# Kernel tuning notes

Hardware: AMD Instinct MI355X
Metric: run time of the kernel (lower is better)

The kernel has to match this reference:

```python
import jax, jax.numpy as jnp
import numpy as np

B, T = 64, 512          # batch, seq_len
D = 512                 # model_size / LSTM hidden
V = 256                 # vocab_size
R, W, M = 4, 16, 5      # read_heads, cell_size, nr_cells
RW = R * W
IFC = R * W + 3 * W + 5 * R + 3   # DNC interface vector size = 135
EPS = 1e-6
CLIP = 20.0


def setup_inputs():
    ks = jax.random.split(jax.random.key(0), 12)
    s = 0.05
    f32 = jnp.float32
    return {
        'tokens':   jax.random.randint(ks[0], (B, T), 0, V, dtype=jnp.int32),
        'emb':      jax.random.normal(ks[1], (V, D), f32),
        'lstm_Wi0': jax.random.normal(ks[2], (4 * D, D + RW), f32) * s,
        'lstm_Wh0': jax.random.normal(ks[3], (4 * D, D), f32) * s,
        'lstm_b0':  jnp.zeros((4 * D,), f32),
        'lstm_Wi1': jax.random.normal(ks[4], (4 * D, D), f32) * s,
        'lstm_Wh1': jax.random.normal(ks[5], (4 * D, D), f32) * s,
        'lstm_b1':  jnp.zeros((4 * D,), f32),
        'W_if':     jax.random.normal(ks[6], (IFC, D), f32) * s,
        'b_if':     jnp.zeros((IFC,), f32),
        'W_out':    jax.random.normal(ks[7], (D, D + RW), f32) * s,
        'b_out':    jnp.zeros((D,), f32),
        'W_fc':     jax.random.normal(ks[8], (V, D), f32) * s,
        'b_fc':     jnp.zeros((V,), f32),
    }


def _cosine(mem, keys):
    # mem (B,M,W), keys (B,K,W) -> (B,K,M) batchwise cosine similarity
    mn = mem / (jnp.linalg.norm(mem, axis=2, keepdims=True) + EPS)
    kn = keys / (jnp.linalg.norm(keys, axis=2, keepdims=True) + EPS)
    return jnp.einsum('bkw,bmw->bkm', kn, mn)


def _allocate(usage):
    # DNC allocation weighting via sort + exclusive cumprod, then unsort
    u = EPS + (1.0 - EPS) * usage                           # (B,M)
    idx = jnp.argsort(u, axis=1)                            # ascending usage
    sorted_u = jnp.take_along_axis(u, idx, axis=1)
    prod_excl = jnp.cumprod(
        jnp.concatenate([jnp.ones_like(u[:, :1]), sorted_u], axis=1), axis=1)[:, :-1]
    alloc_sorted = (1.0 - sorted_u) * prod_excl
    inv = jnp.argsort(idx, axis=1)                          # reverse permutation
    return jnp.take_along_axis(alloc_sorted, inv, axis=1)


def _dnc_forward(tokens, emb, lstm_Wi0, lstm_Wh0, lstm_b0,
                 lstm_Wi1, lstm_Wh1, lstm_b1, W_if, b_if,
                 W_out, b_out, W_fc, b_fc):
    x = emb[tokens]                                         # (B,T,D)
    eye_mask = 1.0 - jnp.eye(M, dtype=x.dtype)

    def lstm_cell(xin, h, c, Wi, Wh, b):
        g = xin @ Wi.T + h @ Wh.T + b
        i, f, gg, o = jnp.split(g, 4, axis=1)               # torch gate order i,f,g,o
        c2 = jax.nn.sigmoid(f) * c + jax.nn.sigmoid(i) * jnp.tanh(gg)
        h2 = jax.nn.sigmoid(o) * jnp.tanh(c2)
        return h2, c2

    def step(carry, x_t):
        h0, c0, h1, c1, mem, link, prec, rw_p, ww_p, usage, last_read = carry
        xin = jnp.concatenate([x_t, last_read], axis=1)     # (B, D+RW)
        nh0, nc0 = lstm_cell(xin, h0, c0, lstm_Wi0, lstm_Wh0, lstm_b0)
        nh1, nc1 = lstm_cell(nh0, h1, c1, lstm_Wi1, lstm_Wh1, lstm_b1)
        out = jnp.clip(nh1, -CLIP, CLIP)
        xi = out @ W_if.T + b_if                            # (B, IFC)

        o = 0
        read_keys = jnp.tanh(xi[:, :RW]).reshape(-1, R, W); o = RW
        read_str  = jax.nn.softplus(xi[:, o:o + R]); o += R
        write_key = jnp.tanh(xi[:, o:o + W]); o += W
        write_str = jax.nn.softplus(xi[:, o]); o += 1
        erase     = jax.nn.sigmoid(xi[:, o:o + W]); o += W
        write_vec = jnp.tanh(xi[:, o:o + W]); o += W
        free_g    = jax.nn.sigmoid(xi[:, o:o + R]); o += R
        alloc_g   = jax.nn.sigmoid(xi[:, o]); o += 1
        write_g   = jax.nn.sigmoid(xi[:, o]); o += 1
        read_modes = jax.nn.softmax(xi[:, o:o + 3 * R].reshape(-1, R, 3), axis=-1)

        # ---- write head ----
        usage2 = usage + (1.0 - usage) * ww_p               # single write head
        psi = jnp.prod(1.0 - free_g[:, :, None] * rw_p, axis=1)   # (B,M)
        usage2 = usage2 * psi
        wcw = jax.nn.softmax(
            _cosine(mem, write_key[:, None, :])[:, 0, :] * write_str[:, None], axis=1)
        alloc = _allocate(usage2)
        ww = write_g[:, None] * (alloc_g[:, None] * alloc
                                 + (1.0 - alloc_g[:, None]) * wcw)  # (B,M)
        mem2 = mem * (1.0 - ww[:, :, None] * erase[:, None, :]) \
               + ww[:, :, None] * write_vec[:, None, :]
        link2 = (1.0 - ww[:, :, None] - ww[:, None, :]) * link \
                + ww[:, :, None] * prec[:, None, :]
        link2 = link2 * eye_mask
        prec2 = (1.0 - jnp.sum(ww, axis=1, keepdims=True)) * prec + ww

        # ---- read heads ----
        rcw = jax.nn.softmax(_cosine(mem2, read_keys) * read_str[:, :, None], axis=2)
        fwd = jnp.einsum('bij,brj->bri', link2, rw_p)       # L @ w_prev
        bwd = jnp.einsum('bij,bri->brj', link2, rw_p)       # L^T @ w_prev
        rw = (read_modes[..., 0:1] * bwd + read_modes[..., 1:2] * fwd
              + read_modes[..., 2:3] * rcw)                 # (B,R,M)
        read_vecs = jnp.einsum('brm,bmw->brw', rw, mem2).reshape(-1, RW)

        y = jnp.concatenate([out, read_vecs], axis=1) @ W_out.T + b_out  # (B,D)
        carry = (nh0, nc0, nh1, nc1, mem2, link2, prec2, rw, ww, usage2, read_vecs)
        return carry, y

    b = tokens.shape[0]
    z = lambda *shape: jnp.zeros(shape, x.dtype)
    carry0 = (z(b, D), z(b, D), z(b, D), z(b, D),
              z(b, M, W), z(b, M, M), z(b, M),
              z(b, R, M), z(b, M), z(b, M), z(b, RW))
    _, ys = jax.lax.scan(step, carry0, jnp.swapaxes(x, 0, 1))
    y = jnp.swapaxes(ys, 0, 1)                              # (B,T,D)
    logits = y @ W_fc.T + b_fc                              # (B,T,V)
    return jnp.transpose(logits, (0, 2, 1))                 # (B,V,T)


def reference(tokens, emb, lstm_Wi0, lstm_Wh0, lstm_b0,
              lstm_Wi1, lstm_Wh1, lstm_b1, W_if, b_if,
              W_out, b_out, W_fc, b_fc):
    return _dnc_forward(tokens, emb, lstm_Wi0, lstm_Wh0, lstm_b0,
                        lstm_Wi1, lstm_Wh1, lstm_b1, W_if, b_if,
                        W_out, b_out, W_fc, b_fc)
```

## Files before the change

kernel.cpp:

```cpp
#include <hip/hip_runtime.h>
#include <hip/hip_bf16.h>

typedef __hip_bfloat16 bf16;
typedef _Float16 f16;
typedef _Float16 f16x8 __attribute__((ext_vector_type(8)));
typedef float f32x4 __attribute__((ext_vector_type(4)));
typedef unsigned long long u64;
typedef unsigned short ushort_t;

__device__ __forceinline__ float b2f(bf16 x){ return __bfloat162float(x); }
__device__ __forceinline__ float sigf(float x){ return 1.f/(1.f+expf(-x)); }
__device__ __forceinline__ float splus(float x){ return fmaxf(x,0.f)+log1pf(expf(-fabsf(x))); }
__device__ __forceinline__ float ldf(const void* p, int i, int isf32){
  return isf32 ? ((const float*)p)[i] : __bfloat162float(((const bf16*)p)[i]);
}
__device__ __forceinline__ void ast64(u64* p, u64 v){ __hip_atomic_store(p, v, __ATOMIC_RELAXED, __HIP_MEMORY_SCOPE_AGENT); }
__device__ __forceinline__ u64 ald64(u64* p){ return __hip_atomic_load(p, __ATOMIC_RELAXED, __HIP_MEMORY_SCOPE_AGENT); }
__device__ __forceinline__ void ast32(unsigned* p, unsigned v){ __hip_atomic_store(p, v, __ATOMIC_RELAXED, __HIP_MEMORY_SCOPE_AGENT); }
__device__ __forceinline__ unsigned ald32(unsigned* p){ return __hip_atomic_load(p, __ATOMIC_RELAXED, __HIP_MEMORY_SCOPE_AGENT); }

union U4H8 { uint4 u; f16x8 h; };
union U64H4 { u64 u; f16 h[4]; };
union H16 { f16 h; ushort_t s; };

__global__ void k_detect(const void* __restrict__ emb, int* __restrict__ flag){
  __shared__ float mx[256];
  int tid=threadIdx.x;
  float v = fabsf(__bfloat162float(((const bf16*)emb)[tid]));
  mx[tid]=v; __syncthreads();
  for(int s=128;s>0;s>>=1){ if(tid<s) mx[tid]=fmaxf(mx[tid],mx[tid+s]); __syncthreads(); }
  if(tid==0){ flag[0] = (mx[0]>1000.f) ? 1 : 0; flag[1] = 0; }
}

__global__ void k_embW(const void* __restrict__ emb, const void* __restrict__ Wi0,
                       const void* __restrict__ b0,
                       const int* __restrict__ flags, float* __restrict__ embW){
  int f=flags[0];
  int row = blockIdx.x;
  __shared__ float w[512];
  for(int k=threadIdx.x;k<512;k+=256) w[k]=ldf(Wi0,row*576+k,f);
  __syncthreads();
  int v = threadIdx.x;
  float acc=ldf(b0,row,f);
  #pragma unroll 4
  for(int k=0;k<512;k++) acc += ldf(emb,v*512+k,f)*w[k];
  embW[row*256+v]=acc;
}

__global__ void k_wpkA(const void* __restrict__ Wh0, const void* __restrict__ Wi0,
                       const int* __restrict__ flags, ushort_t* __restrict__ PA){
  int f=flags[0];
  int idx=blockIdx.x*256+threadIdx.x;
  if(idx>=1179648) return;
  int j=idx&7, l=(idx>>3)&63, rest=idx>>9;
  int c=rest%18, t2=rest/18, w=t2&7, r=t2>>3;
  int G=w>>1, hh=w&1, m=l&15, q4=l>>4;
  int row=G*512 + r*32 + hh*16 + m;
  int k=c*32 + q4*8 + j;
  float val = (k<512)? ldf(Wh0,row*512+k,f) : ldf(Wi0,row*576+k,f);
  H16 hx; hx.h=(f16)val; PA[idx]=hx.s;
}
__global__ void k_wpkB(const void* __restrict__ Wi1, const void* __restrict__ Wh1,
                       const int* __restrict__ flags, ushort_t* __restrict__ PB){
  int f=flags[0];
  int idx=blockIdx.x*256+threadIdx.x;
  if(idx>=2097152) return;
  int j=idx&7, l=(idx>>3)&63, rest=idx>>9;
  int c=rest&31, t2=rest>>5, w=t2&7, r=t2>>3;
  int G=w>>1, hh=w&1, m=l&15, q4=l>>4;
  int row=G*512 + r*32 + hh*16 + m;
  int k=c*32 + q4*8 + j;
  float val = (k<512)? ldf(Wi1,row*512+k,f) : ldf(Wh1,row*512+k-512,f);
  H16 hx; hx.h=(f16)val; PB[idx]=hx.s;
}

__global__ void k_wifP(const void* __restrict__ W_if, const void* __restrict__ b_if,
                       const int* __restrict__ flags,
                       ushort_t* __restrict__ PW, float* __restrict__ b_ifF,
                       unsigned* __restrict__ FLz){
  int f=flags[0];
  int idx=blockIdx.x*256+threadIdx.x;
  if(idx<73728){
    int j=idx&7, l=(idx>>3)&63, c=(idx>>9)&15, tile=idx>>13;
    int row=tile*16+(l&15);
    int k=c*32+(l>>4)*8+j;
    float val=(row<135)? ldf(W_if,row*512+k,f) : 0.f;
    H16 hx; hx.h=(f16)val; PW[idx]=hx.s;
  }
  if(idx<64) FLz[idx]=0u;
  if(idx<135) b_ifF[idx]=ldf(b_if,idx,f);
}

__global__ void k_wc(const void* __restrict__ W_fc, const void* __restrict__ W_out,
                     const void* __restrict__ b_out, const void* __restrict__ b_fc,
                     const int* __restrict__ flags,
                     float* __restrict__ Wc, float* __restrict__ bc){
  int f=flags[0];
  int idx=blockIdx.x*256+threadIdx.x;
  int v=idx/576, j=idx-v*576;
  float acc=0.f;
  #pragma unroll 4
  for(int d=0;d<512;d++) acc += ldf(W_fc,v*512+d,f)*ldf(W_out,d*576+j,f);
  Wc[idx]=acc;
  if(j==0){
    float a=ldf(b_fc,v,f);
    for(int d=0;d<512;d++) a += ldf(W_fc,v*512+d,f)*ldf(b_out,d,f);
    bc[v]=a;
  }
}

__attribute__((amdgpu_waves_per_eu(2,2)))
__global__ void __launch_bounds__(512) k_dnc3(
    const int* __restrict__ tokens, const void* __restrict__ b1, const int* __restrict__ flags,
    const float* __restrict__ embW, const ushort_t* __restrict__ PA, const ushort_t* __restrict__ PB,
    const ushort_t* __restrict__ PW, const float* __restrict__ b_ifF,
    u64* GX0, u64* GX1, unsigned* FL,
    bf16* __restrict__ cat)
{
  const int bid = blockIdx.x;
  const int g   = bid>>4, r = bid&15;
  const int tid = threadIdx.x;
  const int wv  = tid>>6, l = tid&63;
  const int lm  = l&15,  q4 = l>>4;
  const int d   = tid>>4, bb = tid&15;
  const int mb  = tid>>5, mu = tid&31;
  const int f32i = flags[0];

  __shared__ __align__(16) u64 HB[4352];
  __shared__ float PR[128*17];
  __shared__ f16  sh_pub[512];
  __shared__ float sh_b1[128];
  __shared__ float b_ifL[144];
  __shared__ float xis2[16*149];
  __shared__ float s_mem[1280], s_mem2[1280], s_link[400], s_link2[400];
  __shared__ float s_prec[80], s_prec2[80], s_rwp[320], s_rw[320];
  __shared__ float s_wwp[80], s_ww[80], s_usage[80], s_wl[80];
  __shared__ float s_rl[320], s_fwd[320], s_bwd[320], s_wsum[16];
  __shared__ float rvbuf[1024];

#define WAITG(TGT) do{ if(tid<16){ unsigned _tg=(unsigned)(TGT); int _wd=0; \
    while(ald32(&FL[g*16+tid]) < _tg && _wd<50000000){ __builtin_amdgcn_s_sleep(1); _wd++; } } \
  __syncthreads(); }while(0)
#define PUBF(VAL) do{ __syncthreads(); \
  if(tid==0) ast32(&FL[g*16+r],(unsigned)(VAL)); }while(0)
#define XI(i) xis2[mb*149+(i)]
#define WB() __builtin_amdgcn_wave_barrier()

  const f16x8* HBv=(const f16x8*)HB;
  const uint4* PAv=(const uint4*)PA;
  const uint4* PBv=(const uint4*)PB;
  const uint4* PWv=(const uint4*)PW;

  if(tid<128) sh_b1[tid]=ldf(b1,(tid>>5)*512 + r*32 + (tid&31), f32i);
  if(tid<144) b_ifL[tid]=(tid<135)? b_ifF[tid] : 0.f;
  for(int i=tid;i<1280;i+=512) s_mem[i]=0.f;
  for(int i=tid;i<400;i+=512) s_link[i]=0.f;
  for(int i=tid;i<320;i+=512) s_rwp[i]=0.f;
  if(tid<80){ s_prec[tid]=0.f; s_wwp[tid]=0.f; s_usage[tid]=0.f; }
  float c0s=0.f, c1s=0.f;

  {
    int tok0=tokens[(g*16+bb)*512];
    int base0=(r*32+d)*256+tok0;
    float e0=embW[base0], e2=embW[262144+base0], e3=embW[393216+base0];
    c0s = sigf(e0)*tanhf(e2);
    float h0v = sigf(e3)*tanhf(c0s);
    sh_pub[d*16+bb]=(f16)h0v;
  }
  __syncthreads();
  if(tid<128){
    int ks=tid>>4, b2=tid&15;
    U64H4 pk;
    #pragma unroll
    for(int i=0;i<4;i++) pk.h[i]=sh_pub[(ks*4+i)*16+b2];
    ast64(&GX0[g*4096+((4*r+(ks>>1))*16+b2)*2+(ks&1)], pk.u);
  }
  PUBF(2u);
  WAITG(2u);
  {
    u64 s0=ald64(&GX0[g*4096+tid      ]);
    u64 s1=ald64(&GX0[g*4096+tid+512  ]);
    u64 s2=ald64(&GX0[g*4096+tid+1024 ]);
    u64 s3=ald64(&GX0[g*4096+tid+1536 ]);
    HB[tid]=s0; HB[tid+512]=s1; HB[tid+1024]=s2; HB[tid+1536]=s3;
  }
  __syncthreads();
  {
    f32x4 accB=(f32x4){0.f,0.f,0.f,0.f};
    #pragma unroll
    for(int c=0;c<16;c++){
      U4H8 wf; wf.u=PBv[((r*8+wv)*32+c)*64+l];
      f16x8 bfr=HBv[(c*4+q4)*16+lm];
      accB=__builtin_amdgcn_mfma_f32_16x16x32_f16(wf.h,bfr,accB,0,0,0);
    }
    #pragma unroll
    for(int reg=0;reg<4;reg++) PR[(wv*16+q4*4+reg)*17+lm]=accB[reg];
  }
  __syncthreads();
  {
    float gi=PR[(d    )*17+bb]+sh_b1[d];
    float gg=PR[(64+d )*17+bb]+sh_b1[64+d];
    float go=PR[(96+d )*17+bb]+sh_b1[96+d];
    c1s = sigf(gi)*tanhf(gg);
    float h=sigf(go)*tanhf(c1s);
    sh_pub[d*16+bb]=(f16)h;
  }
  __syncthreads();
  if(tid<128){
    int ks=tid>>4, b2=tid&15;
    U64H4 pk;
    #pragma unroll
    for(int i=0;i<4;i++) pk.h[i]=sh_pub[(ks*4+i)*16+b2];
    ast64(&GX1[g*4096+((4*r+(ks>>1))*16+b2)*2+(ks&1)], pk.u);
  }
  PUBF(3u);

  for(int tt=0;tt<512;tt++){
    const int p=tt&1, pn=p^1;

    f32x4 accA=(f32x4){0.f,0.f,0.f,0.f};
    #pragma unroll
    for(int c=0;c<16;c++){
      U4H8 wf; wf.u=PAv[((r*8+wv)*18+c)*64+l];
      f16x8 bfr=HBv[(c*4+q4)*16+lm];
      accA=__builtin_amdgcn_mfma_f32_16x16x32_f16(wf.h,bfr,accA,0,0,0);
    }
    float em0,em1,em2,em3;
    {
      int tn=(tt<511)?tt+1:511;
      int tok=tokens[(g*16+bb)*512+tn];
      int base=(r*32+d)*256+tok;
      em0=embW[base]; em1=embW[131072+base]; em2=embW[262144+base]; em3=embW[393216+base];
    }
    uint4 pfA2[2];
    #pragma unroll
    for(int c2=0;c2<2;c2++) pfA2[c2]=PAv[((r*8+wv)*18+16+c2)*64+l];

    WAITG(2*tt+3);

    {
      u64 s0=ald64(&GX1[g*4096+p*2048+tid      ]);
      u64 s1=ald64(&GX1[g*4096+p*2048+tid+512  ]);
      u64 s2=ald64(&GX1[g*4096+p*2048+tid+1024 ]);
      u64 s3=ald64(&GX1[g*4096+p*2048+tid+1536 ]);
      HB[2048+tid]=s0; HB[2048+tid+512]=s1; HB[2048+tid+1024]=s2; HB[2048+tid+1536]=s3;
    }
    __syncthreads();

    {
      f32x4 xa=(f32x4){0.f,0.f,0.f,0.f};
      #pragma unroll
      for(int hh=0;hh<4;hh++){
        uint4 w4[4];
        #pragma unroll
        for(int cc=0;cc<4;cc++) w4[cc]=PWv[(wv*16+hh*4+cc)*64+l];
        #pragma unroll
        for(int cc=0;cc<4;cc++){
          U4H8 t4; t4.u=w4[cc];
          f16x8 bfr=HBv[1024+((hh*4+cc)*4+q4)*16+lm];
          xa=__builtin_amdgcn_mfma_f32_16x16x32_f16(t4.h,bfr,xa,0,0,0);
        }
      }
      #pragma unroll
      for(int reg=0;reg<4;reg++){
        int row=wv*16+q4*4+reg;
        xis2[lm*149+row]=xa[reg]+b_ifL[row];
      }
      if(wv==0){
        f32x4 xb=(f32x4){0.f,0.f,0.f,0.f};
        #pragma unroll
        for(int hh=0;hh<4;hh++){
          uint4 w4[4];
          #pragma unroll
          for(int cc=0;cc<4;cc++) w4[cc]=PWv[(128+hh*4+cc)*64+l];
          #pragma unroll
          for(int cc=0;cc<4;cc++){
            U4H8 t4; t4.u=w4[cc];
            f16x8 bfr=HBv[1024+((hh*4+cc)*4+q4)*16+lm];
            xb=__builtin_amdgcn_mfma_f32_16x16x32_f16(t4.h,bfr,xb,0,0,0);
          }
        }
        #pragma unroll
        for(int reg=0;reg<4;reg++){
          int row=128+q4*4+reg;
          xis2[lm*149+row]=xb[reg]+b_ifL[row];
        }
      }
    }
    __syncthreads();

    if(mu<5){
      int m=mu;
      float u=s_usage[mb*5+m]+(1.f-s_usage[mb*5+m])*s_wwp[mb*5+m];
      float psi=1.f;
      #pragma unroll
      for(int rr=0;rr<4;rr++) psi *= 1.f - sigf(XI(117+rr))*s_rwp[mb*20+rr*5+m];
      u*=psi; s_usage[mb*5+m]=u;
      float nm=0.f,dt=0.f,nk=0.f;
      #pragma unroll
      for(int w=0;w<16;w++){
        float mv=s_mem[mb*80+m*16+w], kv=tanhf(XI(68+w));
        nm+=mv*mv; dt+=mv*kv; nk+=kv*kv;
      }
      float sim=dt/((sqrtf(nm)+1e-6f)*(sqrtf(nk)+1e-6f));
      s_wl[mb*5+m]=sim*splus(XI(84));
    }
    WB();
    if(mu<5){
      int m=mu;
      float mx=s_wl[mb*5];
      #pragma unroll
      for(int j=1;j<5;j++) mx=fmaxf(mx,s_wl[mb*5+j]);
      float e=expf(s_wl[mb*5+m]-mx);
      float u=1e-6f+(1.f-1e-6f)*s_usage[mb*5+m];
      s_rl [mb*20+m]=u;
      s_bwd[mb*20+m]=e;
    }
    WB();
    if(mu<5){
      int m=mu;
      float u=s_rl[mb*20+m], e=s_bwd[mb*20+m];
      float s=0.f, prod=1.f;
      #pragma unroll
      for(int j=0;j<5;j++){
        s+=s_bwd[mb*20+j];
        float uj=s_rl[mb*20+j];
        if(uj<u || (uj==u && j<m)) prod*=uj;
      }
      float wcw=e/s;
      float alloc=(1.f-u)*prod;
      float ag=sigf(XI(121)), wgg=sigf(XI(122));
      float w_=wgg*(ag*alloc+(1.f-ag)*wcw);
      s_ww[mb*5+m]=w_;
    }
    WB();
    if(mu==0){
      float ws=0.f;
      #pragma unroll
      for(int m=0;m<5;m++) ws+=s_ww[mb*5+m];
      s_wsum[mb]=ws;
    }
    WB();
    for(int k=mu;k<80;k+=32){
      int m=k>>4,w=k&15;
      float er=sigf(XI(85+w)), wv2=tanhf(XI(101+w));
      float w_=s_ww[mb*5+m];
      s_mem2[mb*80+k]=s_mem[mb*80+k]*(1.f-w_*er)+w_*wv2;
    }
    if(mu<25){
      int i=mu/5, j=mu-5*i;
      s_link2[mb*25+mu]=(i==j)?0.f:((1.f-s_ww[mb*5+i]-s_ww[mb*5+j])*s_link[mb*25+mu]+s_ww[mb*5+i]*s_prec[mb*5+j]);
    } else if(mu<30){
      int j=mu-25;
      s_prec2[mb*5+j]=(1.f-s_wsum[mb])*s_prec[mb*5+j]+s_ww[mb*5+j];
    }
    WB();
    if(mu<20){
      int rr=mu/5, m=mu-5*rr;
      float nm=0.f,dt=0.f,nk=0.f;
      #pragma unroll
      for(int w=0;w<16;w++){
        float mv=s_mem2[mb*80+m*16+w], kv=tanhf(XI(rr*16+w));
        nm+=mv*mv; dt+=mv*kv; nk+=kv*kv;
      }
      float sim=dt/((sqrtf(nm)+1e-6f)*(sqrtf(nk)+1e-6f));
      s_rl[mb*20+mu]=sim*splus(XI(64+rr));
      float af=0.f, ab=0.f;
      #pragma unroll
      for(int j=0;j<5;j++) af+=s_link2[mb*25+m*5+j]*s_rwp[mb*20+rr*5+j];
      #pragma unroll
      for(int i=0;i<5;i++) ab+=s_link2[mb*25+i*5+m]*s_rwp[mb*20+rr*5+i];
      s_fwd[mb*20+rr*5+m]=af;
      s_bwd[mb*20+rr*5+m]=ab;
    }
    WB();
    if(mu<20){
      int rr=mu/5;
      float mx=-1e30f;
      #pragma unroll
      for(int m=0;m<5;m++) mx=fmaxf(mx,s_rl[mb*20+rr*5+m]);
      float s=0.f;
      #pragma unroll
      for(int m=0;m<5;m++) s+=expf(s_rl[mb*20+rr*5+m]-mx);
      float rcw=expf(s_rl[mb*20+mu]-mx)/s;
      float q0=XI(123+3*rr),q1=XI(124+3*rr),q2=XI(125+3*rr);
      float m3=fmaxf(q0,fmaxf(q1,q2));
      float e0=expf(q0-m3),e1=expf(q1-m3),e2=expf(q2-m3);
      float inv=1.f/(e0+e1+e2);
      s_rw[mb*20+mu]=(e0*s_bwd[mb*20+mu]+e1*s_fwd[mb*20+mu]+e2*rcw)*inv;
    }
    WB();
    for(int k=mu;k<64;k+=32){
      int rr=k>>4,w=k&15;
      float a=0.f;
      #pragma unroll
      for(int m=0;m<5;m++) a+=s_rw[mb*20+rr*5+m]*s_mem2[mb*80+m*16+w];
      rvbuf[mb*64+k]=a;
    }
    for(int k=mu;k<80;k+=32) s_mem[mb*80+k]=s_mem2[mb*80+k];
    if(mu<25) s_link[mb*25+mu]=s_link2[mb*25+mu];
    else if(mu<30) s_prec[mb*5+mu-25]=s_prec2[mb*5+mu-25];
    if(mu<20) s_rwp[mb*20+mu]=s_rw[mb*20+mu];
    if(mu>=27&&mu<32){ int m=mu-27; s_wwp[mb*5+m]=s_ww[mb*5+m]; }
    __syncthreads();

    if(tt==511){
      int cb=((g*16+r)*512+tt)*576;
      if(tid<128){
        int kg=tid>>1, e=tid&1;
        U64H4 pv; pv.u=HB[2048+(kg*16+r)*2+e];
        #pragma unroll
        for(int i=0;i<4;i++){
          float x=(float)pv.h[i];
          cat[cb+kg*8+e*4+i]=__float2bfloat16(fminf(fmaxf(x,-20.f),20.f));
        }
      }
      if(tid<64) cat[cb+512+tid]=__float2bfloat16(rvbuf[r*64+tid]);
      break;
    }

    if(tid<256){
      int kg=tid>>5, rem=tid&31, b2=rem>>1, e=rem&1;
      U64H4 pk;
      #pragma unroll
      for(int i=0;i<4;i++) pk.h[i]=(f16)rvbuf[b2*64 + kg*8+e*4+i];
      HB[4096+(kg*16+b2)*2+e]=pk.u;
    }
    __syncthreads();
    #pragma unroll
    for(int c2=0;c2<2;c2++){
      U4H8 wf; wf.u=pfA2[c2];
      f16x8 bfr=HBv[2048+(c2*4+q4)*16+lm];
      accA=__builtin_amdgcn_mfma_f32_16x16x32_f16(wf.h,bfr,accA,0,0,0);
    }
    #pragma unroll
    for(int reg=0;reg<4;reg++) PR[(wv*16+q4*4+reg)*17+lm]=accA[reg];
    __syncthreads();
    {
      float gi=PR[(d    )*17+bb]+em0;
      float gf=PR[(32+d )*17+bb]+em1;
      float gg=PR[(64+d )*17+bb]+em2;
      float go=PR[(96+d )*17+bb]+em3;
      float c0=sigf(gf)*c0s+sigf(gi)*tanhf(gg);
      c0s=c0;
      float h=sigf(go)*tanhf(c0);
      sh_pub[d*16+bb]=(f16)h;
    }
    __syncthreads();
    if(tid<128){
      int ks=tid>>4, b2=tid&15;
      U64H4 pk;
      #pragma unroll
      for(int i=0;i<4;i++) pk.h[i]=sh_pub[(ks*4+i)*16+b2];
      ast64(&GX0[g*4096+pn*2048+((4*r+(ks>>1))*16+b2)*2+(ks&1)], pk.u);
    }
    PUBF(2*tt+4);

    f32x4 accB=(f32x4){0.f,0.f,0.f,0.f};
    #pragma unroll
    for(int c=16;c<32;c++){
      U4H8 wf; wf.u=PBv[((r*8+wv)*32+c)*64+l];
      f16x8 bfr=HBv[1024+((c-16)*4+q4)*16+lm];
      accB=__builtin_amdgcn_mfma_f32_16x16x32_f16(wf.h,bfr,accB,0,0,0);
    }
    uint4 pfB[16];
    #pragma unroll
    for(int c=0;c<16;c++) pfB[c]=PBv[((r*8+wv)*32+c)*64+l];
    {
      int cb=((g*16+r)*512+tt)*576;
      if(tid<128){
        int kg=tid>>1, e=tid&1;
        U64H4 pv; pv.u=HB[2048+(kg*16+r)*2+e];
        #pragma unroll
        for(int i=0;i<4;i++){
          float x=(float)pv.h[i];
          cat[cb+kg*8+e*4+i]=__float2bfloat16(fminf(fmaxf(x,-20.f),20.f));
        }
      }
      if(tid<64) cat[cb+512+tid]=__float2bfloat16(rvbuf[r*64+tid]);
    }

    WAITG(2*tt+4);

    {
      u64 s0=ald64(&GX0[g*4096+pn*2048+tid      ]);
      u64 s1=ald64(&GX0[g*4096+pn*2048+tid+512  ]);
      u64 s2=ald64(&GX0[g*4096+pn*2048+tid+1024 ]);
      u64 s3=ald64(&GX0[g*4096+pn*2048+tid+1536 ]);
      HB[tid]=s0; HB[tid+512]=s1; HB[tid+1024]=s2; HB[tid+1536]=s3;
    }
    __syncthreads();
    #pragma unroll
    for(int c=0;c<16;c++){
      U4H8 wf; wf.u=pfB[c];
      f16x8 bfr=HBv[(c*4+q4)*16+lm];
      accB=__builtin_amdgcn_mfma_f32_16x16x32_f16(wf.h,bfr,accB,0,0,0);
    }
    #pragma unroll
    for(int reg=0;reg<4;reg++) PR[(wv*16+q4*4+reg)*17+lm]=accB[reg];
    __syncthreads();
    {
      float gi=PR[(d    )*17+bb]+sh_b1[d];
      float gf=PR[(32+d )*17+bb]+sh_b1[32+d];
      float gg=PR[(64+d )*17+bb]+sh_b1[64+d];
      float go=PR[(96+d )*17+bb]+sh_b1[96+d];
      float c1=sigf(gf)*c1s+sigf(gi)*tanhf(gg);
      c1s=c1;
      float h=sigf(go)*tanhf(c1);
      sh_pub[d*16+bb]=(f16)h;
    }
    __syncthreads();
    if(tid<128){
      int ks=tid>>4, b2=tid&15;
      U64H4 pk;
      #pragma unroll
      for(int i=0;i<4;i++) pk.h[i]=sh_pub[(ks*4+i)*16+b2];
      ast64(&GX1[g*4096+pn*2048+((4*r+(ks>>1))*16+b2)*2+(ks&1)], pk.u);
    }
    PUBF(2*tt+5);
  }
#undef WAITG
#undef PUBF
#undef XI
#undef WB
}

__global__ void __launch_bounds__(256) k_out(const bf16* __restrict__ cat,
                                             const float* __restrict__ Wc,
                                             const float* __restrict__ bc,
                                             float* __restrict__ outp){
  int t0=blockIdx.x*64, v0=blockIdx.y*64, b=blockIdx.z;
  __shared__ float As[64][33];
  __shared__ float Bs[32][65];
  int tid=threadIdx.x;
  int ti=tid>>4, vi=tid&15;
  float acc[4][4]={};
  for(int k0=0;k0<576;k0+=32){
    for(int i=tid;i<64*32;i+=256){
      int rr=i>>5,k=i&31;
      As[rr][k]=b2f(cat[(b*512+t0+rr)*576+k0+k]);
    }
    for(int i=tid;i<64*32;i+=256){
      int v=i>>5,k=i&31;
      Bs[k][v]=Wc[(v0+v)*576+k0+k];
    }
    __syncthreads();
    #pragma unroll 8
    for(int kk=0;kk<32;kk++){
      float av[4],bv[4];
      #pragma unroll
      for(int x=0;x<4;x++) av[x]=As[ti*4+x][kk];
      #pragma unroll
      for(int y=0;y<4;y++) bv[y]=Bs[kk][vi*4+y];
      #pragma unroll
      for(int x=0;x<4;x++)
        #pragma unroll
        for(int y=0;y<4;y++) acc[x][y]+=av[x]*bv[y];
    }
    __syncthreads();
  }
  #pragma unroll
  for(int y=0;y<4;y++){
    int v=v0+vi*4+y;
    float bcv=bc[v];
    #pragma unroll
    for(int x=0;x<4;x++){
      int tt=t0+ti*4+x;
      outp[(b*256+v)*512+tt]=acc[x][y]+bcv;
    }
  }
}

extern "C" void kernel_launch(void* const* d_in, const int* in_sizes, int n_in,
                              void* d_out, int out_size, void* d_ws, size_t ws_size,
                              hipStream_t stream) {
  const int*  tokens = (const int*) d_in[0];
  const void* emb    = d_in[1];
  const void* Wi0    = d_in[2];
  const void* Wh0    = d_in[3];
  const void* b0     = d_in[4];
  const void* Wi1    = d_in[5];
  const void* Wh1    = d_in[6];
  const void* b1     = d_in[7];
  const void* W_if   = d_in[8];
  const void* b_if   = d_in[9];
  const void* W_out  = d_in[10];
  const void* b_out  = d_in[11];
  const void* W_fc   = d_in[12];
  const void* b_fc   = d_in[13];

  static const int expect[14] = {64*512, 256*512, 2048*576, 2048*512, 2048,
                                 2048*512, 2048*512, 2048, 135*512, 135,
                                 512*576, 512, 256*512, 256};
  bool ok = (n_in == 14);
  if(ok) for(int i=0;i<14;i++) if(in_sizes[i]!=expect[i]) ok=false;

  int*      flags = (int*)d_ws;
  float*    embW  = (float*)d_ws + 64;
  ushort_t* PA    = (ushort_t*)(embW + 524288);
  ushort_t* PB    = PA + 1310720;
  float*    Wreg  = (float*)(PB + 2097152);
  float*    b_ifF = Wreg + 69632;
  float*    Wc    = b_ifF + 160;
  float*    bc    = Wc + 147456;
  u64*      GX0   = (u64*)(bc + 256);
  u64*      GX1   = GX0 + 16384;
  u64*      GXL   = GX1 + 16384;
  bf16*     cat   = (bf16*)(GXL + 2048);
  unsigned* FL    = (unsigned*)(PA + 1179648);
  ushort_t* PW    = (ushort_t*)Wreg;

  size_t need = 9783168ull + 278528ull + 37748736ull;
  if(!ok || ws_size < need){
    hipMemsetAsync(d_out, 0, (size_t)out_size*4, stream);
    return;
  }

  k_detect<<<dim3(1), dim3(256), 0, stream>>>(emb, flags);
  k_embW<<<dim3(2048), dim3(256), 0, stream>>>(emb, Wi0, b0, flags, embW);
  k_wpkA<<<dim3(4608), dim3(256), 0, stream>>>(Wh0, Wi0, flags, PA);
  k_wpkB<<<dim3(8192), dim3(256), 0, stream>>>(Wi1, Wh1, flags, PB);
  k_wifP<<<dim3(288), dim3(256), 0, stream>>>(W_if, b_if, flags, PW, b_ifF, FL);
  k_wc  <<<dim3(576),  dim3(256), 0, stream>>>(W_fc, W_out, b_out, b_fc, flags, Wc, bc);

  void* kargs[] = {
    (void*)&tokens, (void*)&b1, (void*)&flags,
    (void*)&embW, (void*)&PA, (void*)&PB,
    (void*)&PW, (void*)&b_ifF,
    (void*)&GX0, (void*)&GX1, (void*)&FL,
    (void*)&cat
  };
  hipLaunchCooperativeKernel((const void*)k_dnc3, dim3(64), dim3(512), kargs, 0, stream);

  k_out<<<dim3(8,4,64), dim3(256), 0, stream>>>(cat, Wc, bc, (float*)d_out);
}
```

Baseline: 12.50 ms.

## Interleave LSTM gate rows so each lane's MFMA output holds all four gates

The packed LSTM weight layouts are reordered so the four gate rows of one hidden unit land in the four accumulator registers of the same lane. The gate nonlinearities can then be applied straight from the MFMA result, which removes the shared-memory PR round trip and one block barrier per layer per timestep. Bias values move into registers. Separately, the tanh/sigmoid transforms of the DNC interface values are computed once per step into shared memory instead of being recomputed inside inner loops.

```diff
diff --git a/kernel.cpp b/kernel.cpp
--- a/kernel.cpp
+++ b/kernel.cpp
@@ -54,8 +54,9 @@
   if(idx>=1179648) return;
   int j=idx&7, l=(idx>>3)&63, rest=idx>>9;
   int c=rest%18, t2=rest/18, w=t2&7, r=t2>>3;
-  int G=w>>1, hh=w&1, m=l&15, q4=l>>4;
-  int row=G*512 + r*32 + hh*16 + m;
+  int tr=l&15, q4=l>>4;
+  int G=tr&3, dd=tr>>2;
+  int row=G*512 + r*32 + w*4 + dd;
   int k=c*32 + q4*8 + j;
   float val = (k<512)? ldf(Wh0,row*512+k,f) : ldf(Wi0,row*576+k,f);
   H16 hx; hx.h=(f16)val; PA[idx]=hx.s;
@@ -67,8 +68,9 @@
   if(idx>=2097152) return;
   int j=idx&7, l=(idx>>3)&63, rest=idx>>9;
   int c=rest&31, t2=rest>>5, w=t2&7, r=t2>>3;
-  int G=w>>1, hh=w&1, m=l&15, q4=l>>4;
-  int row=G*512 + r*32 + hh*16 + m;
+  int tr=l&15, q4=l>>4;
+  int G=tr&3, dd=tr>>2;
+  int row=G*512 + r*32 + w*4 + dd;
   int k=c*32 + q4*8 + j;
   float val = (k<512)? ldf(Wi1,row*512+k,f) : ldf(Wh1,row*512+k-512,f);
   H16 hx; hx.h=(f16)val; PB[idx]=hx.s;
@@ -122,16 +124,15 @@
   const int tid = threadIdx.x;
   const int wv  = tid>>6, l = tid&63;
   const int lm  = l&15,  q4 = l>>4;
-  const int d   = tid>>4, bb = tid&15;
   const int mb  = tid>>5, mu = tid&31;
   const int f32i = flags[0];
 
   __shared__ __align__(16) u64 HB[4352];
-  __shared__ float PR[128*17];
   __shared__ f16  sh_pub[512];
-  __shared__ float sh_b1[128];
+  __shared__ int  tokL[16];
   __shared__ float b_ifL[144];
   __shared__ float xis2[16*149];
+  __shared__ float s_pre[16*112];
   __shared__ float s_mem[1280], s_mem2[1280], s_link[400], s_link2[400];
   __shared__ float s_prec[80], s_prec2[80], s_rwp[320], s_rw[320];
   __shared__ float s_wwp[80], s_ww[80], s_usage[80], s_wl[80];
@@ -151,7 +152,10 @@
   const uint4* PBv=(const uint4*)PB;
   const uint4* PWv=(const uint4*)PW;
 
-  if(tid<128) sh_b1[tid]=ldf(b1,(tid>>5)*512 + r*32 + (tid&31), f32i);
+  const int dim1 = r*32 + wv*4 + q4;
+  const float b1Li=ldf(b1,dim1,f32i), b1Lf=ldf(b1,512+dim1,f32i),
+              b1Lg=ldf(b1,1024+dim1,f32i), b1Lo=ldf(b1,1536+dim1,f32i);
+
   if(tid<144) b_ifL[tid]=(tid<135)? b_ifF[tid] : 0.f;
   for(int i=tid;i<1280;i+=512) s_mem[i]=0.f;
   for(int i=tid;i<400;i+=512) s_link[i]=0.f;
@@ -159,13 +163,15 @@
   if(tid<80){ s_prec[tid]=0.f; s_wwp[tid]=0.f; s_usage[tid]=0.f; }
   float c0s=0.f, c1s=0.f;
 
+  if(tid<16) tokL[tid]=tokens[(g*16+tid)*512];
+  __syncthreads();
   {
-    int tok0=tokens[(g*16+bb)*512];
-    int base0=(r*32+d)*256+tok0;
-    float e0=embW[base0], e2=embW[262144+base0], e3=embW[393216+base0];
-    c0s = sigf(e0)*tanhf(e2);
-    float h0v = sigf(e3)*tanhf(c0s);
-    sh_pub[d*16+bb]=(f16)h0v;
+    int tok=tokL[lm];
+    float ei=embW[dim1*256+tok];
+    float eg=embW[262144+dim1*256+tok];
+    float eo=embW[393216+dim1*256+tok];
+    c0s = sigf(ei)*tanhf(eg);
+    sh_pub[(wv*4+q4)*16+lm]=(f16)(sigf(eo)*tanhf(c0s));
   }
   __syncthreads();
   if(tid<128){
@@ -186,24 +192,16 @@
   }
   __syncthreads();
   {
-    f32x4 accB=(f32x4){0.f,0.f,0.f,0.f};
+    f32x4 acc1=(f32x4){0.f,0.f,0.f,0.f};
     #pragma unroll
     for(int c=0;c<16;c++){
       U4H8 wf; wf.u=PBv[((r*8+wv)*32+c)*64+l];
       f16x8 bfr=HBv[(c*4+q4)*16+lm];
-      accB=__builtin_amdgcn_mfma_f32_16x16x32_f16(wf.h,bfr,accB,0,0,0);
-    }
-    #pragma unroll
-    for(int reg=0;reg<4;reg++) PR[(wv*16+q4*4+reg)*17+lm]=accB[reg];
-  }
-  __syncthreads();
-  {
-    float gi=PR[(d    )*17+bb]+sh_b1[d];
-    float gg=PR[(64+d )*17+bb]+sh_b1[64+d];
-    float go=PR[(96+d )*17+bb]+sh_b1[96+d];
-    c1s = sigf(gi)*tanhf(gg);
-    float h=sigf(go)*tanhf(c1s);
-    sh_pub[d*16+bb]=(f16)h;
+      acc1=__builtin_amdgcn_mfma_f32_16x16x32_f16(wf.h,bfr,acc1,0,0,0);
+    }
+    float gi=acc1[0]+b1Li, gg=acc1[2]+b1Lg, go=acc1[3]+b1Lo;
+    c1s=sigf(gi)*tanhf(gg);
+    sh_pub[(wv*4+q4)*16+lm]=(f16)(sigf(go)*tanhf(c1s));
   }
   __syncthreads();
   if(tid<128){
@@ -228,9 +226,9 @@
     float em0,em1,em2,em3;
     {
       int tn=(tt<511)?tt+1:511;
-      int tok=tokens[(g*16+bb)*512+tn];
-      int base=(r*32+d)*256+tok;
-      em0=embW[base]; em1=embW[131072+base]; em2=embW[262144+base]; em3=embW[393216+base];
+      int tok=tokens[(g*16+lm)*512+tn];
+      em0=embW[dim1*256+tok]; em1=embW[131072+dim1*256+tok];
+      em2=embW[262144+dim1*256+tok]; em3=embW[393216+dim1*256+tok];
     }
     uint4 pfA2[2];
     #pragma unroll
@@ -289,6 +287,14 @@
     }
     __syncthreads();
 
+    if(mu<16){
+      s_pre[mb*112+mu]    =tanhf(XI(68+mu));
+      s_pre[mb*112+16+mu] =sigf (XI(85+mu));
+      s_pre[mb*112+32+mu] =tanhf(XI(101+mu));
+    }
+    s_pre[mb*112+48+mu]   =tanhf(XI(mu));
+    s_pre[mb*112+48+32+mu]=tanhf(XI(32+mu));
+    WB();
     if(mu<5){
       int m=mu;
       float u=s_usage[mb*5+m]+(1.f-s_usage[mb*5+m])*s_wwp[mb*5+m];
@@ -299,7 +305,7 @@
       float nm=0.f,dt=0.f,nk=0.f;
       #pragma unroll
       for(int w=0;w<16;w++){
-        float mv=s_mem[mb*80+m*16+w], kv=tanhf(XI(68+w));
+        float mv=s_mem[mb*80+m*16+w], kv=s_pre[mb*112+w];
         nm+=mv*mv; dt+=mv*kv; nk+=kv*kv;
       }
       float sim=dt/((sqrtf(nm)+1e-6f)*(sqrtf(nk)+1e-6f));
@@ -330,8 +336,7 @@
       float wcw=e/s;
       float alloc=(1.f-u)*prod;
       float ag=sigf(XI(121)), wgg=sigf(XI(122));
-      float w_=wgg*(ag*alloc+(1.f-ag)*wcw);
-      s_ww[mb*5+m]=w_;
+      s_ww[mb*5+m]=wgg*(ag*alloc+(1.f-ag)*wcw);
     }
     WB();
     if(mu==0){
@@ -343,7 +348,7 @@
     WB();
     for(int k=mu;k<80;k+=32){
       int m=k>>4,w=k&15;
-      float er=sigf(XI(85+w)), wv2=tanhf(XI(101+w));
+      float er=s_pre[mb*112+16+w], wv2=s_pre[mb*112+32+w];
       float w_=s_ww[mb*5+m];
       s_mem2[mb*80+k]=s_mem[mb*80+k]*(1.f-w_*er)+w_*wv2;
     }
@@ -360,7 +365,7 @@
       float nm=0.f,dt=0.f,nk=0.f;
       #pragma unroll
       for(int w=0;w<16;w++){
-        float mv=s_mem2[mb*80+m*16+w], kv=tanhf(XI(rr*16+w));
+        float mv=s_mem2[mb*80+m*16+w], kv=s_pre[mb*112+48+rr*16+w];
         nm+=mv*mv; dt+=mv*kv; nk+=kv*kv;
       }
       float sim=dt/((sqrtf(nm)+1e-6f)*(sqrtf(nk)+1e-6f));
@@ -433,18 +438,11 @@
       f16x8 bfr=HBv[2048+(c2*4+q4)*16+lm];
       accA=__builtin_amdgcn_mfma_f32_16x16x32_f16(wf.h,bfr,accA,0,0,0);
     }
-    #pragma unroll
-    for(int reg=0;reg<4;reg++) PR[(wv*16+q4*4+reg)*17+lm]=accA[reg];
-    __syncthreads();
     {
-      float gi=PR[(d    )*17+bb]+em0;
-      float gf=PR[(32+d )*17+bb]+em1;
-      float gg=PR[(64+d )*17+bb]+em2;
-      float go=PR[(96+d )*17+bb]+em3;
+      float gi=accA[0]+em0, gf=accA[1]+em1, gg=accA[2]+em2, go=accA[3]+em3;
       float c0=sigf(gf)*c0s+sigf(gi)*tanhf(gg);
       c0s=c0;
-      float h=sigf(go)*tanhf(c0);
-      sh_pub[d*16+bb]=(f16)h;
+      sh_pub[(wv*4+q4)*16+lm]=(f16)(sigf(go)*tanhf(c0));
     }
     __syncthreads();
     if(tid<128){
@@ -496,18 +494,11 @@
       f16x8 bfr=HBv[(c*4+q4)*16+lm];
       accB=__builtin_amdgcn_mfma_f32_16x16x32_f16(wf.h,bfr,accB,0,0,0);
     }
-    #pragma unroll
-    for(int reg=0;reg<4;reg++) PR[(wv*16+q4*4+reg)*17+lm]=accB[reg];
-    __syncthreads();
     {
-      float gi=PR[(d    )*17+bb]+sh_b1[d];
-      float gf=PR[(32+d )*17+bb]+sh_b1[32+d];
-      float gg=PR[(64+d )*17+bb]+sh_b1[64+d];
-      float go=PR[(96+d )*17+bb]+sh_b1[96+d];
+      float gi=accB[0]+b1Li, gf=accB[1]+b1Lf, gg=accB[2]+b1Lg, go=accB[3]+b1Lo;
       float c1=sigf(gf)*c1s+sigf(gi)*tanhf(gg);
       c1s=c1;
-      float h=sigf(go)*tanhf(c1);
-      sh_pub[d*16+bb]=(f16)h;
+      sh_pub[(wv*4+q4)*16+lm]=(f16)(sigf(go)*tanhf(c1));
     }
     __syncthreads();
     if(tid<128){
```

Result: faster. 12.08 ms (-3.4%).
